# Kernel tuning notes

Hardware: AMD Instinct MI355X
Metric: run time of the kernel (lower is better)

## Reference

```python
import jax, jax.numpy as jnp
import numpy as np

SCALE = 1.0  # std of the Normal error model (init arg `scale`)
B, P, D, T = 32, 256, 64, 4096


def setup_inputs() -> dict:
    key = jax.random.key(0)
    k1, k2, k3 = jax.random.split(key, 3)
    data = jax.random.normal(k1, (B, P, D), dtype=jnp.float32)
    targets = jax.random.normal(k2, (B, P), dtype=jnp.float32)
    task_pool = jax.random.normal(k3, (T, D, 1), dtype=jnp.float32)
    return {"data": data, "targets": targets, "task_pool": task_pool}


def reference(data, targets, task_pool):
    # W: (n_dims, n_tasks), matching task_pool.squeeze(-1).T in the original
    W = task_pool[..., 0].T
    dt = data.dtype

    # Per-point, per-task predictions and Gaussian log-likelihoods, computed ONCE.
    # The original recomputes X@W and the log-prob sum for every prefix i (O(n^2));
    # here a single cumsum over the point axis reproduces the same prefix sums.
    pred_per_task = jnp.einsum('bpd,dt->bpt', data, W)          # (B, P, T)
    err = targets[..., None] - pred_per_task                     # (B, P, T)
    log_norm = -jnp.log(jnp.asarray(SCALE, dt)) - 0.5 * jnp.log(jnp.asarray(2.0 * np.pi, dt))
    scores = -0.5 * (err / SCALE) ** 2 + log_norm                # Normal(0, scale).log_prob

    cum = jnp.cumsum(scores, axis=1)                             # cum[:, i] = sum_{j<=i}
    # Posterior for predicting point i uses points 0..i-1; point 0 uses a uniform
    # posterior (original: W.mean(dim=1) == softmax(zeros) @ W.T).
    log_lik = jnp.concatenate([jnp.zeros_like(cum[:, :1]), cum[:, :-1]], axis=1)
    post = jax.nn.softmax(log_lik, axis=-1)                      # (B, P, T)

    w_mmse = jnp.einsum('bpt,dt->bpd', post, W)                  # posterior-mean weights
    return jnp.einsum('bpd,bpd->bp', data, w_mmse)               # (B, P)
```

## Files before the change

kernel.cpp:

```cpp
#include <hip/hip_runtime.h>
#include <hip/hip_bf16.h>
#include <math.h>

#define Bb 32
#define Pp 256
#define Dd 64
#define Tt 4096

typedef unsigned short ushort_t;
typedef __attribute__((ext_vector_type(8))) short bf16x8;
typedef __attribute__((ext_vector_type(4))) float f32x4;

#define TRIP_BYTES ((size_t)Bb * Pp * 64 * 16)
#define A_BF_BYTES ((size_t)Bb * Pp * Dd * 2)
#define B_BF_BYTES ((size_t)Tt * Dd * 2)
#define WS_NEED    (TRIP_BYTES + 2 * A_BF_BYTES + 2 * B_BF_BYTES)

template <int CTRL>
__device__ __forceinline__ float dppf(float x) {
  return __builtin_bit_cast(float,
      __builtin_amdgcn_update_dpp(0, __builtin_bit_cast(int, x), CTRL, 0xF, 0xF, true));
}

__device__ __forceinline__ f32x4 mfma6(bf16x8 ah0, bf16x8 ah1, bf16x8 al0, bf16x8 al1,
                                       bf16x8 bh0, bf16x8 bh1, bf16x8 bl0, bf16x8 bl1) {
  f32x4 a = (f32x4)0.f;
  a = __builtin_amdgcn_mfma_f32_16x16x32_bf16(ah0, bh0, a, 0, 0, 0);
  a = __builtin_amdgcn_mfma_f32_16x16x32_bf16(ah1, bh1, a, 0, 0, 0);
  a = __builtin_amdgcn_mfma_f32_16x16x32_bf16(ah0, bl0, a, 0, 0, 0);
  a = __builtin_amdgcn_mfma_f32_16x16x32_bf16(al0, bh0, a, 0, 0, 0);
  a = __builtin_amdgcn_mfma_f32_16x16x32_bf16(ah1, bl1, a, 0, 0, 0);
  a = __builtin_amdgcn_mfma_f32_16x16x32_bf16(al1, bh1, a, 0, 0, 0);
  return a;
}

__global__ __launch_bounds__(256) void k_conv(const float* __restrict__ data,
                                              const float* __restrict__ Wt,
                                              ushort_t* __restrict__ Ah, ushort_t* __restrict__ Al,
                                              ushort_t* __restrict__ Bh, ushort_t* __restrict__ Bl) {
  const int i  = blockIdx.x * 256 + threadIdx.x;
  const int NA = Bb * Pp * Dd;
  const float x = (i < NA) ? data[i] : Wt[i - NA];
  const __hip_bfloat16 h = __float2bfloat16(x);
  const float hf = __bfloat162float(h);
  const __hip_bfloat16 l = __float2bfloat16(x - hf);
  if (i < NA) { Ah[i] = *(const ushort_t*)&h; Al[i] = *(const ushort_t*)&l; }
  else        { const int j = i - NA;
                Bh[j] = *(const ushort_t*)&h; Bl[j] = *(const ushort_t*)&l; }
}

__global__ __launch_bounds__(256, 2) void k_main(const ushort_t* __restrict__ Ah,
                                                 const ushort_t* __restrict__ Al,
                                                 const ushort_t* __restrict__ Bh,
                                                 const ushort_t* __restrict__ Bl,
                                                 const float* __restrict__ targets,
                                                 float4* __restrict__ triples) {
  const int tid  = threadIdx.x;
  const int wid  = tid >> 6;
  const int lane = tid & 63;
  const int quad = lane >> 4;
  const int l16  = lane & 15;
  const int b     = blockIdx.x >> 4;
  const int strip = blockIdx.x & 15;
  const int t0    = strip * 256;
  const int wstrip = strip * 4 + wid;

  bf16x8 vbh0[4], vbh1[4], vbl0[4], vbl1[4];
#pragma unroll
  for (int nt = 0; nt < 4; ++nt) {
    const size_t boff = (size_t)(t0 + wid * 64 + nt * 16 + l16) * Dd + quad * 8;
    vbh0[nt] = *(const bf16x8*)(Bh + boff);
    vbh1[nt] = *(const bf16x8*)(Bh + boff + 32);
    vbl0[nt] = *(const bf16x8*)(Bl + boff);
    vbl1[nt] = *(const bf16x8*)(Bl + boff + 32);
  }

  const ushort_t* arow_base = Ah + (size_t)b * Pp * Dd;
  const ushort_t* alow_base = Al + (size_t)b * Pp * Dd;
  float4* __restrict__ trb  = triples + (size_t)b * Pp * 64;

  float R[4];
#pragma unroll
  for (int nt = 0; nt < 4; ++nt) R[nt] = 0.f;

  const size_t aoff0 = (size_t)l16 * Dd + quad * 8;
  bf16x8 ah0 = *(const bf16x8*)(arow_base + aoff0);
  bf16x8 ah1 = *(const bf16x8*)(arow_base + aoff0 + 32);
  bf16x8 al0 = *(const bf16x8*)(alow_base + aoff0);
  bf16x8 al1 = *(const bf16x8*)(alow_base + aoff0 + 32);
  float4 tq  = *(const float4*)(targets + b * Pp + quad * 4);

#pragma unroll 1
  for (int sg = 0; sg < 16; ++sg) {
    const int pn = ((sg + 1) & 15) * 16;
    const size_t an = (size_t)(pn + l16) * Dd + quad * 8;
    const bf16x8 nah0 = *(const bf16x8*)(arow_base + an);
    const bf16x8 nah1 = *(const bf16x8*)(arow_base + an + 32);
    const bf16x8 nal0 = *(const bf16x8*)(alow_base + an);
    const bf16x8 nal1 = *(const bf16x8*)(alow_base + an + 32);
    const float4 ntq  = *(const float4*)(targets + b * Pp + pn + quad * 4);

    float cc[4][4], av[4][4];
#pragma unroll
    for (int nt = 0; nt < 4; ++nt) {
      const f32x4 a = mfma6(ah0, ah1, al0, al1,
                            vbh0[nt], vbh1[nt], vbl0[nt], vbl1[nt]);
      float sc[4];
      { const float e = tq.x - a[0]; sc[0] = -0.5f * e * e; }
      { const float e = tq.y - a[1]; sc[1] = -0.5f * e * e; }
      { const float e = tq.z - a[2]; sc[2] = -0.5f * e * e; }
      { const float e = tq.w - a[3]; sc[3] = -0.5f * e * e; }

      const float colsum = (sc[0] + sc[1]) + (sc[2] + sc[3]);
      const float x1 = __shfl_xor(colsum, 16, 64);
      const float x2 = __shfl_xor(colsum, 32, 64);
      const float x3 = __shfl_xor(x1, 32, 64);
      const float pre = (quad == 0) ? 0.f
                      : (quad == 1) ? x1
                      : (quad == 2) ? (x2 + x3)
                                    : (x1 + x2 + x3);
      const float base = R[nt] + pre;
      cc[nt][0] = base;
      cc[nt][1] = base + sc[0];
      cc[nt][2] = cc[nt][1] + sc[1];
      cc[nt][3] = cc[nt][2] + sc[2];
#pragma unroll
      for (int r = 0; r < 4; ++r) av[nt][r] = a[r];

      R[nt] += ((colsum + x1) + (x2 + x3));
    }

    float mm[4], ss[4], vv[4];
#pragma unroll
    for (int r = 0; r < 4; ++r) {
      const float m01 = fmaxf(cc[0][r], cc[1][r]);
      const float m23 = fmaxf(cc[2][r], cc[3][r]);
      mm[r] = fmaxf(m01, m23);
      float s = 0.f, v = 0.f;
#pragma unroll
      for (int nt = 0; nt < 4; ++nt) {
        const float e = __expf(cc[nt][r] - mm[r]);
        s += e;
        v = fmaf(e, av[nt][r], v);
      }
      ss[r] = s; vv[r] = v;
    }

    float M[4];
#pragma unroll
    for (int r = 0; r < 4; ++r) M[r] = mm[r];
#pragma unroll
    for (int r = 0; r < 4; ++r) M[r] = fmaxf(M[r], dppf<0xB1>(M[r]));
#pragma unroll
    for (int r = 0; r < 4; ++r) M[r] = fmaxf(M[r], dppf<0x4E>(M[r]));
#pragma unroll
    for (int r = 0; r < 4; ++r) M[r] = fmaxf(M[r], dppf<0x141>(M[r]));
#pragma unroll
    for (int r = 0; r < 4; ++r) M[r] = fmaxf(M[r], dppf<0x140>(M[r]));
#pragma unroll
    for (int r = 0; r < 4; ++r) {
      const float f = __expf(mm[r] - M[r]);
      ss[r] *= f; vv[r] *= f;
    }
#pragma unroll
    for (int r = 0; r < 4; ++r) { ss[r] += dppf<0xB1>(ss[r]);  vv[r] += dppf<0xB1>(vv[r]); }
#pragma unroll
    for (int r = 0; r < 4; ++r) { ss[r] += dppf<0x4E>(ss[r]);  vv[r] += dppf<0x4E>(vv[r]); }
#pragma unroll
    for (int r = 0; r < 4; ++r) { ss[r] += dppf<0x141>(ss[r]); vv[r] += dppf<0x141>(vv[r]); }
#pragma unroll
    for (int r = 0; r < 4; ++r) { ss[r] += dppf<0x140>(ss[r]); vv[r] += dppf<0x140>(vv[r]); }

    if (l16 == 0) {
#pragma unroll
      for (int r = 0; r < 4; ++r) {
        const int p = sg * 16 + quad * 4 + r;
        trb[p * 64 + wstrip] = make_float4(M[r], ss[r], vv[r], 0.f);
      }
    }

    ah0 = nah0; ah1 = nah1; al0 = nal0; al1 = nal1; tq = ntq;
  }
}

__global__ __launch_bounds__(256) void k_merge(const float4* __restrict__ ws,
                                               float* __restrict__ out) {
  const int gt   = blockIdx.x * 256 + threadIdx.x;
  const int bp   = gt >> 6;
  const int lane = gt & 63;
  const float4 o = ws[(size_t)bp * 64 + lane];
  const float m = o.x, s = o.y, v = o.z;
  float M = m;
#pragma unroll
  for (int off = 32; off; off >>= 1) M = fmaxf(M, __shfl_xor(M, off, 64));
  const float f = __expf(m - M);
  float S = f * s, V = f * v;
#pragma unroll
  for (int off = 32; off; off >>= 1) {
    S += __shfl_xor(S, off, 64);
    V += __shfl_xor(V, off, 64);
  }
  if (lane == 0) out[bp] = V / S;
}

__global__ __launch_bounds__(256) void k_scan_fused(const float* __restrict__ data,
                                                    const float* __restrict__ targets,
                                                    const float* __restrict__ task_pool,
                                                    float4* __restrict__ ws) {
  const int b     = blockIdx.x >> 4;
  const int wid   = threadIdx.x >> 6;
  const int lane  = threadIdx.x & 63;
  const int chunk = ((blockIdx.x & 15) << 2) | wid;
  const int t     = (chunk << 6) | lane;
  float w[Dd];
#pragma unroll
  for (int d = 0; d < Dd; d += 4) {
    const float4 r = *(const float4*)(task_pool + (size_t)t * Dd + d);
    w[d] = r.x; w[d + 1] = r.y; w[d + 2] = r.z; w[d + 3] = r.w;
  }
  const float* drow = data + (size_t)b * (Pp * Dd);
  const float* tgt  = targets + b * Pp;
  float4* wsb       = ws + (size_t)b * (Pp * 64);
  float c = 0.f;
  for (int p = 0; p < Pp; ++p) {
    float a0 = 0.f, a1 = 0.f, a2 = 0.f, a3 = 0.f;
    const float* r = drow + p * Dd;
#pragma unroll
    for (int d = 0; d < Dd; d += 4) {
      a0 = fmaf(r[d], w[d], a0);         a1 = fmaf(r[d + 1], w[d + 1], a1);
      a2 = fmaf(r[d + 2], w[d + 2], a2); a3 = fmaf(r[d + 3], w[d + 3], a3);
    }
    const float pred = (a0 + a1) + (a2 + a3);
    float m = c;
#pragma unroll
    for (int off = 32; off; off >>= 1) m = fmaxf(m, __shfl_xor(m, off, 64));
    const float e = __expf(c - m);
    float s = e, v = e * pred;
#pragma unroll
    for (int off = 32; off; off >>= 1) {
      s += __shfl_xor(s, off, 64);
      v += __shfl_xor(v, off, 64);
    }
    if (lane == 0) wsb[p * 64 + chunk] = make_float4(m, s, v, 0.f);
    const float err = tgt[p] - pred;
    c = fmaf(-0.5f * err, err, c);
  }
}

extern "C" void kernel_launch(void* const* d_in, const int* in_sizes, int n_in,
                              void* d_out, int out_size, void* d_ws, size_t ws_size,
                              hipStream_t stream) {
  const float* data      = (const float*)d_in[0];
  const float* targets   = (const float*)d_in[1];
  const float* task_pool = (const float*)d_in[2];
  float* out = (float*)d_out;

  if (ws_size >= WS_NEED) {
    float4*   trips = (float4*)d_ws;
    char*     cb    = (char*)d_ws + TRIP_BYTES;
    ushort_t* Ah    = (ushort_t*)cb;
    ushort_t* Al    = (ushort_t*)(cb + A_BF_BYTES);
    ushort_t* Bh    = (ushort_t*)(cb + 2 * A_BF_BYTES);
    ushort_t* Bl    = (ushort_t*)(cb + 2 * A_BF_BYTES + B_BF_BYTES);
    k_conv <<<dim3((Bb * Pp * Dd + Tt * Dd) / 256), dim3(256), 0, stream>>>(
        data, task_pool, Ah, Al, Bh, Bl);
    k_main <<<dim3(Bb * 16), dim3(256), 0, stream>>>(Ah, Al, Bh, Bl, targets, trips);
    k_merge<<<dim3((Bb * Pp * 64) / 256), dim3(256), 0, stream>>>(trips, out);
  } else {
    float4* triples = (float4*)d_ws;
    k_scan_fused<<<dim3(512), dim3(256), 0, stream>>>(data, targets, task_pool, triples);
    k_merge<<<dim3((Bb * Pp * 64) / 256), dim3(256), 0, stream>>>(triples, out);
  }
}
```

Baseline: 101.0 us.

## Fuse bf16 split conversion into main kernel and split point scan across two blocks

Result: slower. 187.9 us (+86.0%).

```diff
diff --git a/kernel.cpp b/kernel.cpp
--- a/kernel.cpp
+++ b/kernel.cpp
@@ -12,9 +12,17 @@
 typedef __attribute__((ext_vector_type(4))) float f32x4;
 
 #define TRIP_BYTES ((size_t)Bb * Pp * 64 * 16)
-#define A_BF_BYTES ((size_t)Bb * Pp * Dd * 2)
-#define B_BF_BYTES ((size_t)Tt * Dd * 2)
-#define WS_NEED    (TRIP_BYTES + 2 * A_BF_BYTES + 2 * B_BF_BYTES)
+#define WS_NEED    TRIP_BYTES
+
+#define C2 (-0.7213475204444817f)
+
+__device__ __forceinline__ float fexp2(float x) {
+#if __has_builtin(__builtin_amdgcn_exp2f)
+  return __builtin_amdgcn_exp2f(x);
+#else
+  float r; asm("v_exp_f32 %0, %1" : "=v"(r) : "v"(x)); return r;
+#endif
+}
 
 template <int CTRL>
 __device__ __forceinline__ float dppf(float x) {
@@ -34,152 +42,177 @@
   return a;
 }
 
-__global__ __launch_bounds__(256) void k_conv(const float* __restrict__ data,
-                                              const float* __restrict__ Wt,
-                                              ushort_t* __restrict__ Ah, ushort_t* __restrict__ Al,
-                                              ushort_t* __restrict__ Bh, ushort_t* __restrict__ Bl) {
-  const int i  = blockIdx.x * 256 + threadIdx.x;
-  const int NA = Bb * Pp * Dd;
-  const float x = (i < NA) ? data[i] : Wt[i - NA];
-  const __hip_bfloat16 h = __float2bfloat16(x);
-  const float hf = __bfloat162float(h);
-  const __hip_bfloat16 l = __float2bfloat16(x - hf);
-  if (i < NA) { Ah[i] = *(const ushort_t*)&h; Al[i] = *(const ushort_t*)&l; }
-  else        { const int j = i - NA;
-                Bh[j] = *(const ushort_t*)&h; Bl[j] = *(const ushort_t*)&l; }
-}
-
-__global__ __launch_bounds__(256, 2) void k_main(const ushort_t* __restrict__ Ah,
-                                                 const ushort_t* __restrict__ Al,
-                                                 const ushort_t* __restrict__ Bh,
-                                                 const ushort_t* __restrict__ Bl,
+__device__ __forceinline__ void cvt8(const float4 a, const float4 b,
+                                     bf16x8* hi, bf16x8* lo) {
+  float f[8] = {a.x, a.y, a.z, a.w, b.x, b.y, b.z, b.w};
+  bf16x8 h, l;
+#pragma unroll
+  for (int j = 0; j < 8; ++j) {
+    const __hip_bfloat16 hb = __float2bfloat16(f[j]);
+    const float hf = __bfloat162float(hb);
+    const __hip_bfloat16 lb = __float2bfloat16(f[j] - hf);
+    h[j] = *(const short*)&hb;
+    l[j] = *(const short*)&lb;
+  }
+  *hi = h; *lo = l;
+}
+
+struct TrueC  { static constexpr bool value = true;  };
+struct FalseC { static constexpr bool value = false; };
+
+#define SPLIT 10
+__global__ __launch_bounds__(256, 4) void k_main(const float* __restrict__ data,
                                                  const float* __restrict__ targets,
+                                                 const float* __restrict__ task_pool,
                                                  float4* __restrict__ triples) {
   const int tid  = threadIdx.x;
   const int wid  = tid >> 6;
   const int lane = tid & 63;
   const int quad = lane >> 4;
   const int l16  = lane & 15;
-  const int b     = blockIdx.x >> 4;
-  const int strip = blockIdx.x & 15;
+  const int b     = blockIdx.x >> 5;
+  const int sub   = blockIdx.x & 31;
+  const int strip = sub >> 1;
+  const int half  = sub & 1;
   const int t0    = strip * 256;
   const int wstrip = strip * 4 + wid;
 
   bf16x8 vbh0[4], vbh1[4], vbl0[4], vbl1[4];
 #pragma unroll
   for (int nt = 0; nt < 4; ++nt) {
-    const size_t boff = (size_t)(t0 + wid * 64 + nt * 16 + l16) * Dd + quad * 8;
-    vbh0[nt] = *(const bf16x8*)(Bh + boff);
-    vbh1[nt] = *(const bf16x8*)(Bh + boff + 32);
-    vbl0[nt] = *(const bf16x8*)(Bl + boff);
-    vbl1[nt] = *(const bf16x8*)(Bl + boff + 32);
-  }
-
-  const ushort_t* arow_base = Ah + (size_t)b * Pp * Dd;
-  const ushort_t* alow_base = Al + (size_t)b * Pp * Dd;
-  float4* __restrict__ trb  = triples + (size_t)b * Pp * 64;
+    const float* wr = task_pool + (size_t)(t0 + wid * 64 + nt * 16 + l16) * Dd + quad * 8;
+    const float4 f0 = *(const float4*)(wr);
+    const float4 f1 = *(const float4*)(wr + 4);
+    const float4 f2 = *(const float4*)(wr + 32);
+    const float4 f3 = *(const float4*)(wr + 36);
+    cvt8(f0, f1, &vbh0[nt], &vbl0[nt]);
+    cvt8(f2, f3, &vbh1[nt], &vbl1[nt]);
+  }
+
+  const float* arow = data + (size_t)b * Pp * Dd;
+  const float* tgt  = targets + b * Pp;
+  float4* __restrict__ trb = triples + (size_t)b * Pp * 64;
 
   float R[4];
 #pragma unroll
   for (int nt = 0; nt < 4; ++nt) R[nt] = 0.f;
 
-  const size_t aoff0 = (size_t)l16 * Dd + quad * 8;
-  bf16x8 ah0 = *(const bf16x8*)(arow_base + aoff0);
-  bf16x8 ah1 = *(const bf16x8*)(arow_base + aoff0 + 32);
-  bf16x8 al0 = *(const bf16x8*)(alow_base + aoff0);
-  bf16x8 al1 = *(const bf16x8*)(alow_base + aoff0 + 32);
-  float4 tq  = *(const float4*)(targets + b * Pp + quad * 4);
-
-#pragma unroll 1
-  for (int sg = 0; sg < 16; ++sg) {
+  bf16x8 ah0, ah1, al0, al1;
+  {
+    const size_t a0 = (size_t)l16 * Dd + quad * 8;
+    const float4 f0 = *(const float4*)(arow + a0);
+    const float4 f1 = *(const float4*)(arow + a0 + 4);
+    const float4 f2 = *(const float4*)(arow + a0 + 32);
+    const float4 f3 = *(const float4*)(arow + a0 + 36);
+    cvt8(f0, f1, &ah0, &al0);
+    cvt8(f2, f3, &ah1, &al1);
+  }
+  float4 tq = *(const float4*)(tgt + quad * 4);
+
+  auto step = [&](auto fullc, int sg) {
+    constexpr bool FULL_ = decltype(fullc)::value;
     const int pn = ((sg + 1) & 15) * 16;
     const size_t an = (size_t)(pn + l16) * Dd + quad * 8;
-    const bf16x8 nah0 = *(const bf16x8*)(arow_base + an);
-    const bf16x8 nah1 = *(const bf16x8*)(arow_base + an + 32);
-    const bf16x8 nal0 = *(const bf16x8*)(alow_base + an);
-    const bf16x8 nal1 = *(const bf16x8*)(alow_base + an + 32);
-    const float4 ntq  = *(const float4*)(targets + b * Pp + pn + quad * 4);
+    const float4 nf0 = *(const float4*)(arow + an);
+    const float4 nf1 = *(const float4*)(arow + an + 4);
+    const float4 nf2 = *(const float4*)(arow + an + 32);
+    const float4 nf3 = *(const float4*)(arow + an + 36);
+    const float4 ntq = *(const float4*)(tgt + pn + quad * 4);
 
     float cc[4][4], av[4][4];
 #pragma unroll
     for (int nt = 0; nt < 4; ++nt) {
       const f32x4 a = mfma6(ah0, ah1, al0, al1,
                             vbh0[nt], vbh1[nt], vbl0[nt], vbl1[nt]);
-      float sc[4];
-      { const float e = tq.x - a[0]; sc[0] = -0.5f * e * e; }
-      { const float e = tq.y - a[1]; sc[1] = -0.5f * e * e; }
-      { const float e = tq.z - a[2]; sc[2] = -0.5f * e * e; }
-      { const float e = tq.w - a[3]; sc[3] = -0.5f * e * e; }
-
-      const float colsum = (sc[0] + sc[1]) + (sc[2] + sc[3]);
+      float sc0, sc1, sc2, sc3;
+      { const float e = tq.x - a[0]; sc0 = C2 * e * e; }
+      { const float e = tq.y - a[1]; sc1 = C2 * e * e; }
+      { const float e = tq.z - a[2]; sc2 = C2 * e * e; }
+      { const float e = tq.w - a[3]; sc3 = C2 * e * e; }
+
+      const float colsum = (sc0 + sc1) + (sc2 + sc3);
       const float x1 = __shfl_xor(colsum, 16, 64);
       const float x2 = __shfl_xor(colsum, 32, 64);
       const float x3 = __shfl_xor(x1, 32, 64);
-      const float pre = (quad == 0) ? 0.f
-                      : (quad == 1) ? x1
-                      : (quad == 2) ? (x2 + x3)
-                                    : (x1 + x2 + x3);
-      const float base = R[nt] + pre;
-      cc[nt][0] = base;
-      cc[nt][1] = base + sc[0];
-      cc[nt][2] = cc[nt][1] + sc[1];
-      cc[nt][3] = cc[nt][2] + sc[2];
-#pragma unroll
-      for (int r = 0; r < 4; ++r) av[nt][r] = a[r];
-
+      if (FULL_) {
+        const float pre = (quad == 0) ? 0.f
+                        : (quad == 1) ? x1
+                        : (quad == 2) ? (x2 + x3)
+                                      : (x1 + x2 + x3);
+        const float base = R[nt] + pre;
+        cc[nt][0] = base;
+        cc[nt][1] = base + sc0;
+        cc[nt][2] = cc[nt][1] + sc1;
+        cc[nt][3] = cc[nt][2] + sc2;
+        av[nt][0] = a[0]; av[nt][1] = a[1]; av[nt][2] = a[2]; av[nt][3] = a[3];
+      }
       R[nt] += ((colsum + x1) + (x2 + x3));
     }
 
-    float mm[4], ss[4], vv[4];
-#pragma unroll
-    for (int r = 0; r < 4; ++r) {
-      const float m01 = fmaxf(cc[0][r], cc[1][r]);
-      const float m23 = fmaxf(cc[2][r], cc[3][r]);
-      mm[r] = fmaxf(m01, m23);
-      float s = 0.f, v = 0.f;
-#pragma unroll
-      for (int nt = 0; nt < 4; ++nt) {
-        const float e = __expf(cc[nt][r] - mm[r]);
-        s += e;
-        v = fmaf(e, av[nt][r], v);
-      }
-      ss[r] = s; vv[r] = v;
-    }
-
-    float M[4];
-#pragma unroll
-    for (int r = 0; r < 4; ++r) M[r] = mm[r];
-#pragma unroll
-    for (int r = 0; r < 4; ++r) M[r] = fmaxf(M[r], dppf<0xB1>(M[r]));
-#pragma unroll
-    for (int r = 0; r < 4; ++r) M[r] = fmaxf(M[r], dppf<0x4E>(M[r]));
-#pragma unroll
-    for (int r = 0; r < 4; ++r) M[r] = fmaxf(M[r], dppf<0x141>(M[r]));
-#pragma unroll
-    for (int r = 0; r < 4; ++r) M[r] = fmaxf(M[r], dppf<0x140>(M[r]));
-#pragma unroll
-    for (int r = 0; r < 4; ++r) {
-      const float f = __expf(mm[r] - M[r]);
-      ss[r] *= f; vv[r] *= f;
-    }
-#pragma unroll
-    for (int r = 0; r < 4; ++r) { ss[r] += dppf<0xB1>(ss[r]);  vv[r] += dppf<0xB1>(vv[r]); }
-#pragma unroll
-    for (int r = 0; r < 4; ++r) { ss[r] += dppf<0x4E>(ss[r]);  vv[r] += dppf<0x4E>(vv[r]); }
-#pragma unroll
-    for (int r = 0; r < 4; ++r) { ss[r] += dppf<0x141>(ss[r]); vv[r] += dppf<0x141>(vv[r]); }
-#pragma unroll
-    for (int r = 0; r < 4; ++r) { ss[r] += dppf<0x140>(ss[r]); vv[r] += dppf<0x140>(vv[r]); }
-
-    if (l16 == 0) {
+    if (FULL_) {
+      float mm[4], ss[4], vv[4];
 #pragma unroll
       for (int r = 0; r < 4; ++r) {
-        const int p = sg * 16 + quad * 4 + r;
-        trb[p * 64 + wstrip] = make_float4(M[r], ss[r], vv[r], 0.f);
-      }
-    }
-
-    ah0 = nah0; ah1 = nah1; al0 = nal0; al1 = nal1; tq = ntq;
+        const float m01 = fmaxf(cc[0][r], cc[1][r]);
+        const float m23 = fmaxf(cc[2][r], cc[3][r]);
+        mm[r] = fmaxf(m01, m23);
+        float s = 0.f, v = 0.f;
+#pragma unroll
+        for (int nt = 0; nt < 4; ++nt) {
+          const float e = fexp2(cc[nt][r] - mm[r]);
+          s += e;
+          v = fmaf(e, av[nt][r], v);
+        }
+        ss[r] = s; vv[r] = v;
+      }
+
+      float M[4];
+#pragma unroll
+      for (int r = 0; r < 4; ++r) M[r] = mm[r];
+#pragma unroll
+      for (int r = 0; r < 4; ++r) M[r] = fmaxf(M[r], dppf<0xB1>(M[r]));
+#pragma unroll
+      for (int r = 0; r < 4; ++r) M[r] = fmaxf(M[r], dppf<0x4E>(M[r]));
+#pragma unroll
+      for (int r = 0; r < 4; ++r) M[r] = fmaxf(M[r], dppf<0x141>(M[r]));
+#pragma unroll
+      for (int r = 0; r < 4; ++r) M[r] = fmaxf(M[r], dppf<0x140>(M[r]));
+#pragma unroll
+      for (int r = 0; r < 4; ++r) {
+        const float f = fexp2(mm[r] - M[r]);
+        ss[r] *= f; vv[r] *= f;
+      }
+#pragma unroll
+      for (int r = 0; r < 4; ++r) { ss[r] += dppf<0xB1>(ss[r]);  vv[r] += dppf<0xB1>(vv[r]); }
+#pragma unroll
+      for (int r = 0; r < 4; ++r) { ss[r] += dppf<0x4E>(ss[r]);  vv[r] += dppf<0x4E>(vv[r]); }
+#pragma unroll
+      for (int r = 0; r < 4; ++r) { ss[r] += dppf<0x141>(ss[r]); vv[r] += dppf<0x141>(vv[r]); }
+#pragma unroll
+      for (int r = 0; r < 4; ++r) { ss[r] += dppf<0x140>(ss[r]); vv[r] += dppf<0x140>(vv[r]); }
+
+      if (l16 == 0) {
+#pragma unroll
+        for (int r = 0; r < 4; ++r) {
+          const int p = sg * 16 + quad * 4 + r;
+          trb[p * 64 + wstrip] = make_float4(M[r], ss[r], vv[r], 0.f);
+        }
+      }
+    }
+
+    cvt8(nf0, nf1, &ah0, &al0);
+    cvt8(nf2, nf3, &ah1, &al1);
+    tq = ntq;
+  };
+
+  if (half == 0) {
+#pragma unroll 1
+    for (int sg = 0; sg < SPLIT; ++sg) step(TrueC{}, sg);
+  } else {
+#pragma unroll 1
+    for (int sg = 0; sg < SPLIT; ++sg) step(FalseC{}, sg);
+#pragma unroll 1
+    for (int sg = SPLIT; sg < 16; ++sg) step(TrueC{}, sg);
   }
 }
 
@@ -193,7 +226,7 @@
   float M = m;
 #pragma unroll
   for (int off = 32; off; off >>= 1) M = fmaxf(M, __shfl_xor(M, off, 64));
-  const float f = __expf(m - M);
+  const float f = fexp2(m - M);
   float S = f * s, V = f * v;
 #pragma unroll
   for (int off = 32; off; off >>= 1) {
@@ -234,7 +267,7 @@
     float m = c;
 #pragma unroll
     for (int off = 32; off; off >>= 1) m = fmaxf(m, __shfl_xor(m, off, 64));
-    const float e = __expf(c - m);
+    const float e = fexp2(c - m);
     float s = e, v = e * pred;
 #pragma unroll
     for (int off = 32; off; off >>= 1) {
@@ -243,7 +276,7 @@
     }
     if (lane == 0) wsb[p * 64 + chunk] = make_float4(m, s, v, 0.f);
     const float err = tgt[p] - pred;
-    c = fmaf(-0.5f * err, err, c);
+    c = fmaf(C2 * err, err, c);
   }
 }
 
@@ -255,20 +288,12 @@
   const float* task_pool = (const float*)d_in[2];
   float* out = (float*)d_out;
 
+  float4* trips = (float4*)d_ws;
   if (ws_size >= WS_NEED) {
-    float4*   trips = (float4*)d_ws;
-    char*     cb    = (char*)d_ws + TRIP_BYTES;
-    ushort_t* Ah    = (ushort_t*)cb;
-    ushort_t* Al    = (ushort_t*)(cb + A_BF_BYTES);
-    ushort_t* Bh    = (ushort_t*)(cb + 2 * A_BF_BYTES);
-    ushort_t* Bl    = (ushort_t*)(cb + 2 * A_BF_BYTES + B_BF_BYTES);
-    k_conv <<<dim3((Bb * Pp * Dd + Tt * Dd) / 256), dim3(256), 0, stream>>>(
-        data, task_pool, Ah, Al, Bh, Bl);
-    k_main <<<dim3(Bb * 16), dim3(256), 0, stream>>>(Ah, Al, Bh, Bl, targets, trips);
+    k_main <<<dim3(Bb * 32), dim3(256), 0, stream>>>(data, targets, task_pool, trips);
     k_merge<<<dim3((Bb * Pp * 64) / 256), dim3(256), 0, stream>>>(trips, out);
   } else {
-    float4* triples = (float4*)d_ws;
-    k_scan_fused<<<dim3(512), dim3(256), 0, stream>>>(data, targets, task_pool, triples);
-    k_merge<<<dim3((Bb * Pp * 64) / 256), dim3(256), 0, stream>>>(triples, out);
-  }
-}
+    k_scan_fused<<<dim3(512), dim3(256), 0, stream>>>(data, targets, task_pool, trips);
+    k_merge<<<dim3((Bb * Pp * 64) / 256), dim3(256), 0, stream>>>(trips, out);
+  }
+}
```

## Split point scan across two blocks with redundant prefix recompute; use base-2 exp

Applied to the files above, without the earlier changes.

Measured after the change: 179.0 us. 77.2% more time.

```diff
diff --git a/kernel.cpp b/kernel.cpp
--- a/kernel.cpp
+++ b/kernel.cpp
@@ -15,6 +15,12 @@
 #define A_BF_BYTES ((size_t)Bb * Pp * Dd * 2)
 #define B_BF_BYTES ((size_t)Tt * Dd * 2)
 #define WS_NEED    (TRIP_BYTES + 2 * A_BF_BYTES + 2 * B_BF_BYTES)
+
+#define C2 (-0.7213475204444817f)
+
+__device__ __forceinline__ float fexp2(float x) {
+  float r; asm("v_exp_f32 %0, %1" : "=v"(r) : "v"(x)); return r;
+}
 
 template <int CTRL>
 __device__ __forceinline__ float dppf(float x) {
@@ -49,7 +55,110 @@
                 Bh[j] = *(const ushort_t*)&h; Bl[j] = *(const ushort_t*)&l; }
 }
 
-__global__ __launch_bounds__(256, 2) void k_main(const ushort_t* __restrict__ Ah,
+#define SPLIT 10
+
+template <bool FULL>
+__device__ __forceinline__ void step_fn(
+    int sg, int quad, int l16, int wstrip,
+    const ushort_t* __restrict__ arow_base, const ushort_t* __restrict__ alow_base,
+    const float* __restrict__ tgt, float4* __restrict__ trb,
+    bf16x8& ah0, bf16x8& ah1, bf16x8& al0, bf16x8& al1, float4& tq,
+    float (&R)[4],
+    const bf16x8 (&vbh0)[4], const bf16x8 (&vbh1)[4],
+    const bf16x8 (&vbl0)[4], const bf16x8 (&vbl1)[4]) {
+  const int pn = ((sg + 1) & 15) * 16;
+  const size_t an = (size_t)(pn + l16) * Dd + quad * 8;
+  const bf16x8 nah0 = *(const bf16x8*)(arow_base + an);
+  const bf16x8 nah1 = *(const bf16x8*)(arow_base + an + 32);
+  const bf16x8 nal0 = *(const bf16x8*)(alow_base + an);
+  const bf16x8 nal1 = *(const bf16x8*)(alow_base + an + 32);
+  const float4 ntq  = *(const float4*)(tgt + pn + quad * 4);
+
+  float cc[4][4], av[4][4];
+#pragma unroll
+  for (int nt = 0; nt < 4; ++nt) {
+    const f32x4 a = mfma6(ah0, ah1, al0, al1,
+                          vbh0[nt], vbh1[nt], vbl0[nt], vbl1[nt]);
+    float sc0, sc1, sc2, sc3;
+    { const float e = tq.x - a[0]; sc0 = C2 * e * e; }
+    { const float e = tq.y - a[1]; sc1 = C2 * e * e; }
+    { const float e = tq.z - a[2]; sc2 = C2 * e * e; }
+    { const float e = tq.w - a[3]; sc3 = C2 * e * e; }
+
+    const float colsum = (sc0 + sc1) + (sc2 + sc3);
+    const float x1 = __shfl_xor(colsum, 16, 64);
+    const float x2 = __shfl_xor(colsum, 32, 64);
+    const float x3 = __shfl_xor(x1, 32, 64);
+    if (FULL) {
+      const float pre = (quad == 0) ? 0.f
+                      : (quad == 1) ? x1
+                      : (quad == 2) ? (x2 + x3)
+                                    : (x1 + x2 + x3);
+      const float base = R[nt] + pre;
+      cc[nt][0] = base;
+      cc[nt][1] = base + sc0;
+      cc[nt][2] = cc[nt][1] + sc1;
+      cc[nt][3] = cc[nt][2] + sc2;
+      av[nt][0] = a[0]; av[nt][1] = a[1]; av[nt][2] = a[2]; av[nt][3] = a[3];
+    }
+    R[nt] += ((colsum + x1) + (x2 + x3));
+  }
+
+  if (FULL) {
+    float mm[4], ss[4], vv[4];
+#pragma unroll
+    for (int r = 0; r < 4; ++r) {
+      const float m01 = fmaxf(cc[0][r], cc[1][r]);
+      const float m23 = fmaxf(cc[2][r], cc[3][r]);
+      mm[r] = fmaxf(m01, m23);
+      float s = 0.f, v = 0.f;
+#pragma unroll
+      for (int nt = 0; nt < 4; ++nt) {
+        const float e = fexp2(cc[nt][r] - mm[r]);
+        s += e;
+        v = fmaf(e, av[nt][r], v);
+      }
+      ss[r] = s; vv[r] = v;
+    }
+
+    float M[4];
+#pragma unroll
+    for (int r = 0; r < 4; ++r) M[r] = mm[r];
+#pragma unroll
+    for (int r = 0; r < 4; ++r) M[r] = fmaxf(M[r], dppf<0xB1>(M[r]));
+#pragma unroll
+    for (int r = 0; r < 4; ++r) M[r] = fmaxf(M[r], dppf<0x4E>(M[r]));
+#pragma unroll
+    for (int r = 0; r < 4; ++r) M[r] = fmaxf(M[r], dppf<0x141>(M[r]));
+#pragma unroll
+    for (int r = 0; r < 4; ++r) M[r] = fmaxf(M[r], dppf<0x140>(M[r]));
+#pragma unroll
+    for (int r = 0; r < 4; ++r) {
+      const float f = fexp2(mm[r] - M[r]);
+      ss[r] *= f; vv[r] *= f;
+    }
+#pragma unroll
+    for (int r = 0; r < 4; ++r) { ss[r] += dppf<0xB1>(ss[r]);  vv[r] += dppf<0xB1>(vv[r]); }
+#pragma unroll
+    for (int r = 0; r < 4; ++r) { ss[r] += dppf<0x4E>(ss[r]);  vv[r] += dppf<0x4E>(vv[r]); }
+#pragma unroll
+    for (int r = 0; r < 4; ++r) { ss[r] += dppf<0x141>(ss[r]); vv[r] += dppf<0x141>(vv[r]); }
+#pragma unroll
+    for (int r = 0; r < 4; ++r) { ss[r] += dppf<0x140>(ss[r]); vv[r] += dppf<0x140>(vv[r]); }
+
+    if (l16 == 0) {
+#pragma unroll
+      for (int r = 0; r < 4; ++r) {
+        const int p = sg * 16 + quad * 4 + r;
+        trb[p * 64 + wstrip] = make_float4(M[r], ss[r], vv[r], 0.f);
+      }
+    }
+  }
+
+  ah0 = nah0; ah1 = nah1; al0 = nal0; al1 = nal1; tq = ntq;
+}
+
+__global__ __launch_bounds__(256, 4) void k_main(const ushort_t* __restrict__ Ah,
                                                  const ushort_t* __restrict__ Al,
                                                  const ushort_t* __restrict__ Bh,
                                                  const ushort_t* __restrict__ Bl,
@@ -60,8 +169,10 @@
   const int lane = tid & 63;
   const int quad = lane >> 4;
   const int l16  = lane & 15;
-  const int b     = blockIdx.x >> 4;
-  const int strip = blockIdx.x & 15;
+  const int b     = blockIdx.x >> 5;
+  const int sub   = blockIdx.x & 31;
+  const int strip = sub >> 1;
+  const int half  = sub & 1;
   const int t0    = strip * 256;
   const int wstrip = strip * 4 + wid;
 
@@ -77,6 +188,7 @@
 
   const ushort_t* arow_base = Ah + (size_t)b * Pp * Dd;
   const ushort_t* alow_base = Al + (size_t)b * Pp * Dd;
+  const float* tgt          = targets + b * Pp;
   float4* __restrict__ trb  = triples + (size_t)b * Pp * 64;
 
   float R[4];
@@ -88,98 +200,22 @@
   bf16x8 ah1 = *(const bf16x8*)(arow_base + aoff0 + 32);
   bf16x8 al0 = *(const bf16x8*)(alow_base + aoff0);
   bf16x8 al1 = *(const bf16x8*)(alow_base + aoff0 + 32);
-  float4 tq  = *(const float4*)(targets + b * Pp + quad * 4);
-
+  float4 tq  = *(const float4*)(tgt + quad * 4);
+
+  if (half == 0) {
 #pragma unroll 1
-  for (int sg = 0; sg < 16; ++sg) {
-    const int pn = ((sg + 1) & 15) * 16;
-    const size_t an = (size_t)(pn + l16) * Dd + quad * 8;
-    const bf16x8 nah0 = *(const bf16x8*)(arow_base + an);
-    const bf16x8 nah1 = *(const bf16x8*)(arow_base + an + 32);
-    const bf16x8 nal0 = *(const bf16x8*)(alow_base + an);
-    const bf16x8 nal1 = *(const bf16x8*)(alow_base + an + 32);
-    const float4 ntq  = *(const float4*)(targets + b * Pp + pn + quad * 4);
-
-    float cc[4][4], av[4][4];
-#pragma unroll
-    for (int nt = 0; nt < 4; ++nt) {
-      const f32x4 a = mfma6(ah0, ah1, al0, al1,
-                            vbh0[nt], vbh1[nt], vbl0[nt], vbl1[nt]);
-      float sc[4];
-      { const float e = tq.x - a[0]; sc[0] = -0.5f * e * e; }
-      { const float e = tq.y - a[1]; sc[1] = -0.5f * e * e; }
-      { const float e = tq.z - a[2]; sc[2] = -0.5f * e * e; }
-      { const float e = tq.w - a[3]; sc[3] = -0.5f * e * e; }
-
-      const float colsum = (sc[0] + sc[1]) + (sc[2] + sc[3]);
-      const float x1 = __shfl_xor(colsum, 16, 64);
-      const float x2 = __shfl_xor(colsum, 32, 64);
-      const float x3 = __shfl_xor(x1, 32, 64);
-      const float pre = (quad == 0) ? 0.f
-                      : (quad == 1) ? x1
-                      : (quad == 2) ? (x2 + x3)
-                                    : (x1 + x2 + x3);
-      const float base = R[nt] + pre;
-      cc[nt][0] = base;
-      cc[nt][1] = base + sc[0];
-      cc[nt][2] = cc[nt][1] + sc[1];
-      cc[nt][3] = cc[nt][2] + sc[2];
-#pragma unroll
-      for (int r = 0; r < 4; ++r) av[nt][r] = a[r];
-
-      R[nt] += ((colsum + x1) + (x2 + x3));
-    }
-
-    float mm[4], ss[4], vv[4];
-#pragma unroll
-    for (int r = 0; r < 4; ++r) {
-      const float m01 = fmaxf(cc[0][r], cc[1][r]);
-      const float m23 = fmaxf(cc[2][r], cc[3][r]);
-      mm[r] = fmaxf(m01, m23);
-      float s = 0.f, v = 0.f;
-#pragma unroll
-      for (int nt = 0; nt < 4; ++nt) {
-        const float e = __expf(cc[nt][r] - mm[r]);
-        s += e;
-        v = fmaf(e, av[nt][r], v);
-      }
-      ss[r] = s; vv[r] = v;
-    }
-
-    float M[4];
-#pragma unroll
-    for (int r = 0; r < 4; ++r) M[r] = mm[r];
-#pragma unroll
-    for (int r = 0; r < 4; ++r) M[r] = fmaxf(M[r], dppf<0xB1>(M[r]));
-#pragma unroll
-    for (int r = 0; r < 4; ++r) M[r] = fmaxf(M[r], dppf<0x4E>(M[r]));
-#pragma unroll
-    for (int r = 0; r < 4; ++r) M[r] = fmaxf(M[r], dppf<0x141>(M[r]));
-#pragma unroll
-    for (int r = 0; r < 4; ++r) M[r] = fmaxf(M[r], dppf<0x140>(M[r]));
-#pragma unroll
-    for (int r = 0; r < 4; ++r) {
-      const float f = __expf(mm[r] - M[r]);
-      ss[r] *= f; vv[r] *= f;
-    }
-#pragma unroll
-    for (int r = 0; r < 4; ++r) { ss[r] += dppf<0xB1>(ss[r]);  vv[r] += dppf<0xB1>(vv[r]); }
-#pragma unroll
-    for (int r = 0; r < 4; ++r) { ss[r] += dppf<0x4E>(ss[r]);  vv[r] += dppf<0x4E>(vv[r]); }
-#pragma unroll
-    for (int r = 0; r < 4; ++r) { ss[r] += dppf<0x141>(ss[r]); vv[r] += dppf<0x141>(vv[r]); }
-#pragma unroll
-    for (int r = 0; r < 4; ++r) { ss[r] += dppf<0x140>(ss[r]); vv[r] += dppf<0x140>(vv[r]); }
-
-    if (l16 == 0) {
-#pragma unroll
-      for (int r = 0; r < 4; ++r) {
-        const int p = sg * 16 + quad * 4 + r;
-        trb[p * 64 + wstrip] = make_float4(M[r], ss[r], vv[r], 0.f);
-      }
-    }
-
-    ah0 = nah0; ah1 = nah1; al0 = nal0; al1 = nal1; tq = ntq;
+    for (int sg = 0; sg < SPLIT; ++sg)
+      step_fn<true>(sg, quad, l16, wstrip, arow_base, alow_base, tgt, trb,
+                    ah0, ah1, al0, al1, tq, R, vbh0, vbh1, vbl0, vbl1);
+  } else {
+#pragma unroll 1
+    for (int sg = 0; sg < SPLIT; ++sg)
+      step_fn<false>(sg, quad, l16, wstrip, arow_base, alow_base, tgt, trb,
+                     ah0, ah1, al0, al1, tq, R, vbh0, vbh1, vbl0, vbl1);
+#pragma unroll 1
+    for (int sg = SPLIT; sg < 16; ++sg)
+      step_fn<true>(sg, quad, l16, wstrip, arow_base, alow_base, tgt, trb,
+                    ah0, ah1, al0, al1, tq, R, vbh0, vbh1, vbl0, vbl1);
   }
 }
 
@@ -193,7 +229,7 @@
   float M = m;
 #pragma unroll
   for (int off = 32; off; off >>= 1) M = fmaxf(M, __shfl_xor(M, off, 64));
-  const float f = __expf(m - M);
+  const float f = fexp2(m - M);
   float S = f * s, V = f * v;
 #pragma unroll
   for (int off = 32; off; off >>= 1) {
@@ -234,7 +270,7 @@
     float m = c;
 #pragma unroll
     for (int off = 32; off; off >>= 1) m = fmaxf(m, __shfl_xor(m, off, 64));
-    const float e = __expf(c - m);
+    const float e = fexp2(c - m);
     float s = e, v = e * pred;
 #pragma unroll
     for (int off = 32; off; off >>= 1) {
@@ -243,7 +279,7 @@
     }
     if (lane == 0) wsb[p * 64 + chunk] = make_float4(m, s, v, 0.f);
     const float err = tgt[p] - pred;
-    c = fmaf(-0.5f * err, err, c);
+    c = fmaf(C2 * err, err, c);
   }
 }
 
@@ -264,7 +300,7 @@
     ushort_t* Bl    = (ushort_t*)(cb + 2 * A_BF_BYTES + B_BF_BYTES);
     k_conv <<<dim3((Bb * Pp * Dd + Tt * Dd) / 256), dim3(256), 0, stream>>>(
         data, task_pool, Ah, Al, Bh, Bl);
-    k_main <<<dim3(Bb * 16), dim3(256), 0, stream>>>(Ah, Al, Bh, Bl, targets, trips);
+    k_main <<<dim3(Bb * 32), dim3(256), 0, stream>>>(Ah, Al, Bh, Bl, targets, trips);
     k_merge<<<dim3((Bb * Pp * 64) / 256), dim3(256), 0, stream>>>(trips, out);
   } else {
     float4* triples = (float4*)d_ws;
```

## Halve per-wave task strip, double blocks, compress partials to log-sum-exp pairs

Applied to the files above, without the earlier changes.

Result: slower. 106.8 us (+5.7%).

```diff
diff --git a/kernel.cpp b/kernel.cpp
--- a/kernel.cpp
+++ b/kernel.cpp
@@ -11,10 +11,22 @@
 typedef __attribute__((ext_vector_type(8))) short bf16x8;
 typedef __attribute__((ext_vector_type(4))) float f32x4;
 
-#define TRIP_BYTES ((size_t)Bb * Pp * 64 * 16)
+#define TRIP_BYTES ((size_t)Bb * Pp * 128 * 8)
 #define A_BF_BYTES ((size_t)Bb * Pp * Dd * 2)
 #define B_BF_BYTES ((size_t)Tt * Dd * 2)
 #define WS_NEED    (TRIP_BYTES + 2 * A_BF_BYTES + 2 * B_BF_BYTES)
+
+#define C2 (-0.7213475204444817f)
+
+__device__ __forceinline__ float fexp2(float x) {
+  float r; asm("v_exp_f32 %0, %1" : "=v"(r) : "v"(x)); return r;
+}
+__device__ __forceinline__ float flog2(float x) {
+  float r; asm("v_log_f32 %0, %1" : "=v"(r) : "v"(x)); return r;
+}
+__device__ __forceinline__ float frcp(float x) {
+  float r; asm("v_rcp_f32 %0, %1" : "=v"(r) : "v"(x)); return r;
+}
 
 template <int CTRL>
 __device__ __forceinline__ float dppf(float x) {
@@ -49,69 +61,64 @@
                 Bh[j] = *(const ushort_t*)&h; Bl[j] = *(const ushort_t*)&l; }
 }
 
-__global__ __launch_bounds__(256, 2) void k_main(const ushort_t* __restrict__ Ah,
+__global__ __launch_bounds__(256, 4) void k_main(const ushort_t* __restrict__ Ah,
                                                  const ushort_t* __restrict__ Al,
                                                  const ushort_t* __restrict__ Bh,
                                                  const ushort_t* __restrict__ Bl,
                                                  const float* __restrict__ targets,
-                                                 float4* __restrict__ triples) {
+                                                 float2* __restrict__ trips) {
   const int tid  = threadIdx.x;
   const int wid  = tid >> 6;
   const int lane = tid & 63;
   const int quad = lane >> 4;
   const int l16  = lane & 15;
-  const int b     = blockIdx.x >> 4;
-  const int strip = blockIdx.x & 15;
-  const int t0    = strip * 256;
+  const int b     = blockIdx.x >> 5;
+  const int strip = blockIdx.x & 31;
+  const int t0    = strip * 128;
   const int wstrip = strip * 4 + wid;
 
-  bf16x8 vbh0[4], vbh1[4], vbl0[4], vbl1[4];
-#pragma unroll
-  for (int nt = 0; nt < 4; ++nt) {
-    const size_t boff = (size_t)(t0 + wid * 64 + nt * 16 + l16) * Dd + quad * 8;
-    vbh0[nt] = *(const bf16x8*)(Bh + boff);
-    vbh1[nt] = *(const bf16x8*)(Bh + boff + 32);
-    vbl0[nt] = *(const bf16x8*)(Bl + boff);
-    vbl1[nt] = *(const bf16x8*)(Bl + boff + 32);
+  bf16x8 b0h0, b0h1, b0l0, b0l1, b1h0, b1h1, b1l0, b1l1;
+  {
+    const size_t r0 = (size_t)(t0 + wid * 32 + l16) * Dd + quad * 8;
+    b0h0 = *(const bf16x8*)(Bh + r0);
+    b0h1 = *(const bf16x8*)(Bh + r0 + 32);
+    b0l0 = *(const bf16x8*)(Bl + r0);
+    b0l1 = *(const bf16x8*)(Bl + r0 + 32);
+    const size_t r1 = r0 + (size_t)16 * Dd;
+    b1h0 = *(const bf16x8*)(Bh + r1);
+    b1h1 = *(const bf16x8*)(Bh + r1 + 32);
+    b1l0 = *(const bf16x8*)(Bl + r1);
+    b1l1 = *(const bf16x8*)(Bl + r1 + 32);
   }
 
   const ushort_t* arow_base = Ah + (size_t)b * Pp * Dd;
   const ushort_t* alow_base = Al + (size_t)b * Pp * Dd;
-  float4* __restrict__ trb  = triples + (size_t)b * Pp * 64;
-
-  float R[4];
-#pragma unroll
-  for (int nt = 0; nt < 4; ++nt) R[nt] = 0.f;
-
-  const size_t aoff0 = (size_t)l16 * Dd + quad * 8;
-  bf16x8 ah0 = *(const bf16x8*)(arow_base + aoff0);
-  bf16x8 ah1 = *(const bf16x8*)(arow_base + aoff0 + 32);
-  bf16x8 al0 = *(const bf16x8*)(alow_base + aoff0);
-  bf16x8 al1 = *(const bf16x8*)(alow_base + aoff0 + 32);
-  float4 tq  = *(const float4*)(targets + b * Pp + quad * 4);
+  const float* tgt          = targets + b * Pp;
+  float2* __restrict__ trb  = trips + (size_t)b * Pp * 128;
+
+  float R0 = 0.f, R1 = 0.f;
 
 #pragma unroll 1
   for (int sg = 0; sg < 16; ++sg) {
-    const int pn = ((sg + 1) & 15) * 16;
-    const size_t an = (size_t)(pn + l16) * Dd + quad * 8;
-    const bf16x8 nah0 = *(const bf16x8*)(arow_base + an);
-    const bf16x8 nah1 = *(const bf16x8*)(arow_base + an + 32);
-    const bf16x8 nal0 = *(const bf16x8*)(alow_base + an);
-    const bf16x8 nal1 = *(const bf16x8*)(alow_base + an + 32);
-    const float4 ntq  = *(const float4*)(targets + b * Pp + pn + quad * 4);
-
-    float cc[4][4], av[4][4];
-#pragma unroll
-    for (int nt = 0; nt < 4; ++nt) {
-      const f32x4 a = mfma6(ah0, ah1, al0, al1,
-                            vbh0[nt], vbh1[nt], vbl0[nt], vbl1[nt]);
-      float sc[4];
-      { const float e = tq.x - a[0]; sc[0] = -0.5f * e * e; }
-      { const float e = tq.y - a[1]; sc[1] = -0.5f * e * e; }
-      { const float e = tq.z - a[2]; sc[2] = -0.5f * e * e; }
-      { const float e = tq.w - a[3]; sc[3] = -0.5f * e * e; }
-
-      const float colsum = (sc[0] + sc[1]) + (sc[2] + sc[3]);
+    const int p0 = sg * 16;
+    const size_t aoff = (size_t)(p0 + l16) * Dd + quad * 8;
+    const bf16x8 ah0 = *(const bf16x8*)(arow_base + aoff);
+    const bf16x8 ah1 = *(const bf16x8*)(arow_base + aoff + 32);
+    const bf16x8 al0 = *(const bf16x8*)(alow_base + aoff);
+    const bf16x8 al1 = *(const bf16x8*)(alow_base + aoff + 32);
+    const float4 tq  = *(const float4*)(tgt + p0 + quad * 4);
+
+    const f32x4 a0 = mfma6(ah0, ah1, al0, al1, b0h0, b0h1, b0l0, b0l1);
+    const f32x4 a1 = mfma6(ah0, ah1, al0, al1, b1h0, b1h1, b1l0, b1l1);
+
+    float cc0_0, cc0_1, cc0_2, cc0_3, cc1_0, cc1_1, cc1_2, cc1_3;
+    {
+      float s0, s1, s2, s3;
+      { const float e = tq.x - a0[0]; s0 = C2 * e * e; }
+      { const float e = tq.y - a0[1]; s1 = C2 * e * e; }
+      { const float e = tq.z - a0[2]; s2 = C2 * e * e; }
+      { const float e = tq.w - a0[3]; s3 = C2 * e * e; }
+      const float colsum = (s0 + s1) + (s2 + s3);
       const float x1 = __shfl_xor(colsum, 16, 64);
       const float x2 = __shfl_xor(colsum, 32, 64);
       const float x3 = __shfl_xor(x1, 32, 64);
@@ -119,82 +126,100 @@
                       : (quad == 1) ? x1
                       : (quad == 2) ? (x2 + x3)
                                     : (x1 + x2 + x3);
-      const float base = R[nt] + pre;
-      cc[nt][0] = base;
-      cc[nt][1] = base + sc[0];
-      cc[nt][2] = cc[nt][1] + sc[1];
-      cc[nt][3] = cc[nt][2] + sc[2];
-#pragma unroll
-      for (int r = 0; r < 4; ++r) av[nt][r] = a[r];
-
-      R[nt] += ((colsum + x1) + (x2 + x3));
-    }
-
-    float mm[4], ss[4], vv[4];
-#pragma unroll
-    for (int r = 0; r < 4; ++r) {
-      const float m01 = fmaxf(cc[0][r], cc[1][r]);
-      const float m23 = fmaxf(cc[2][r], cc[3][r]);
-      mm[r] = fmaxf(m01, m23);
-      float s = 0.f, v = 0.f;
-#pragma unroll
-      for (int nt = 0; nt < 4; ++nt) {
-        const float e = __expf(cc[nt][r] - mm[r]);
-        s += e;
-        v = fmaf(e, av[nt][r], v);
+      const float base = R0 + pre;
+      cc0_0 = base;
+      cc0_1 = base + s0;
+      cc0_2 = cc0_1 + s1;
+      cc0_3 = cc0_2 + s2;
+      R0 += ((colsum + x1) + (x2 + x3));
+    }
+    {
+      float s0, s1, s2, s3;
+      { const float e = tq.x - a1[0]; s0 = C2 * e * e; }
+      { const float e = tq.y - a1[1]; s1 = C2 * e * e; }
+      { const float e = tq.z - a1[2]; s2 = C2 * e * e; }
+      { const float e = tq.w - a1[3]; s3 = C2 * e * e; }
+      const float colsum = (s0 + s1) + (s2 + s3);
+      const float x1 = __shfl_xor(colsum, 16, 64);
+      const float x2 = __shfl_xor(colsum, 32, 64);
+      const float x3 = __shfl_xor(x1, 32, 64);
+      const float pre = (quad == 0) ? 0.f
+                      : (quad == 1) ? x1
+                      : (quad == 2) ? (x2 + x3)
+                                    : (x1 + x2 + x3);
+      const float base = R1 + pre;
+      cc1_0 = base;
+      cc1_1 = base + s0;
+      cc1_2 = cc1_1 + s1;
+      cc1_3 = cc1_2 + s2;
+      R1 += ((colsum + x1) + (x2 + x3));
+    }
+
+    float M[4];
+    M[0] = fmaxf(cc0_0, cc1_0);
+    M[1] = fmaxf(cc0_1, cc1_1);
+    M[2] = fmaxf(cc0_2, cc1_2);
+    M[3] = fmaxf(cc0_3, cc1_3);
+#pragma unroll
+    for (int r = 0; r < 4; ++r) M[r] = fmaxf(M[r], dppf<0xB1>(M[r]));
+#pragma unroll
+    for (int r = 0; r < 4; ++r) M[r] = fmaxf(M[r], dppf<0x4E>(M[r]));
+#pragma unroll
+    for (int r = 0; r < 4; ++r) M[r] = fmaxf(M[r], dppf<0x141>(M[r]));
+#pragma unroll
+    for (int r = 0; r < 4; ++r) M[r] = fmaxf(M[r], dppf<0x140>(M[r]));
+
+    float ss[4], vv[4];
+    {
+      const float e0 = fexp2(cc0_0 - M[0]), e1 = fexp2(cc1_0 - M[0]);
+      ss[0] = e0 + e1; vv[0] = fmaf(e0, a0[0], e1 * a1[0]);
+    }
+    {
+      const float e0 = fexp2(cc0_1 - M[1]), e1 = fexp2(cc1_1 - M[1]);
+      ss[1] = e0 + e1; vv[1] = fmaf(e0, a0[1], e1 * a1[1]);
+    }
+    {
+      const float e0 = fexp2(cc0_2 - M[2]), e1 = fexp2(cc1_2 - M[2]);
+      ss[2] = e0 + e1; vv[2] = fmaf(e0, a0[2], e1 * a1[2]);
+    }
+    {
+      const float e0 = fexp2(cc0_3 - M[3]), e1 = fexp2(cc1_3 - M[3]);
+      ss[3] = e0 + e1; vv[3] = fmaf(e0, a0[3], e1 * a1[3]);
+    }
+
+#pragma unroll
+    for (int r = 0; r < 4; ++r) { ss[r] += dppf<0xB1>(ss[r]);  vv[r] += dppf<0xB1>(vv[r]); }
+#pragma unroll
+    for (int r = 0; r < 4; ++r) { ss[r] += dppf<0x4E>(ss[r]);  vv[r] += dppf<0x4E>(vv[r]); }
+#pragma unroll
+    for (int r = 0; r < 4; ++r) { ss[r] += dppf<0x141>(ss[r]); vv[r] += dppf<0x141>(vv[r]); }
+#pragma unroll
+    for (int r = 0; r < 4; ++r) { ss[r] += dppf<0x140>(ss[r]); vv[r] += dppf<0x140>(vv[r]); }
+
+    if (l16 == 0) {
+#pragma unroll
+      for (int r = 0; r < 4; ++r) {
+        const float lm = M[r] + flog2(ss[r]);
+        const float u  = vv[r] * frcp(ss[r]);
+        const int p = p0 + quad * 4 + r;
+        trb[p * 128 + wstrip] = make_float2(lm, u);
       }
-      ss[r] = s; vv[r] = v;
-    }
-
-    float M[4];
-#pragma unroll
-    for (int r = 0; r < 4; ++r) M[r] = mm[r];
-#pragma unroll
-    for (int r = 0; r < 4; ++r) M[r] = fmaxf(M[r], dppf<0xB1>(M[r]));
-#pragma unroll
-    for (int r = 0; r < 4; ++r) M[r] = fmaxf(M[r], dppf<0x4E>(M[r]));
-#pragma unroll
-    for (int r = 0; r < 4; ++r) M[r] = fmaxf(M[r], dppf<0x141>(M[r]));
-#pragma unroll
-    for (int r = 0; r < 4; ++r) M[r] = fmaxf(M[r], dppf<0x140>(M[r]));
-#pragma unroll
-    for (int r = 0; r < 4; ++r) {
-      const float f = __expf(mm[r] - M[r]);
-      ss[r] *= f; vv[r] *= f;
-    }
-#pragma unroll
-    for (int r = 0; r < 4; ++r) { ss[r] += dppf<0xB1>(ss[r]);  vv[r] += dppf<0xB1>(vv[r]); }
-#pragma unroll
-    for (int r = 0; r < 4; ++r) { ss[r] += dppf<0x4E>(ss[r]);  vv[r] += dppf<0x4E>(vv[r]); }
-#pragma unroll
-    for (int r = 0; r < 4; ++r) { ss[r] += dppf<0x141>(ss[r]); vv[r] += dppf<0x141>(vv[r]); }
-#pragma unroll
-    for (int r = 0; r < 4; ++r) { ss[r] += dppf<0x140>(ss[r]); vv[r] += dppf<0x140>(vv[r]); }
-
-    if (l16 == 0) {
-#pragma unroll
-      for (int r = 0; r < 4; ++r) {
-        const int p = sg * 16 + quad * 4 + r;
-        trb[p * 64 + wstrip] = make_float4(M[r], ss[r], vv[r], 0.f);
-      }
-    }
-
-    ah0 = nah0; ah1 = nah1; al0 = nal0; al1 = nal1; tq = ntq;
-  }
-}
-
-__global__ __launch_bounds__(256) void k_merge(const float4* __restrict__ ws,
+    }
+  }
+}
+
+__global__ __launch_bounds__(256) void k_merge(const float2* __restrict__ ws,
                                                float* __restrict__ out) {
-  const int gt   = blockIdx.x * 256 + threadIdx.x;
-  const int bp   = gt >> 6;
-  const int lane = gt & 63;
-  const float4 o = ws[(size_t)bp * 64 + lane];
-  const float m = o.x, s = o.y, v = o.z;
-  float M = m;
+  const int bp   = blockIdx.x * 4 + (threadIdx.x >> 6);
+  const int lane = threadIdx.x & 63;
+  const float2 e0 = ws[(size_t)bp * 128 + lane];
+  const float2 e1 = ws[(size_t)bp * 128 + 64 + lane];
+  float M = fmaxf(e0.x, e1.x);
 #pragma unroll
   for (int off = 32; off; off >>= 1) M = fmaxf(M, __shfl_xor(M, off, 64));
-  const float f = __expf(m - M);
-  float S = f * s, V = f * v;
+  const float f0 = fexp2(e0.x - M), f1 = fexp2(e1.x - M);
+  float S = f0 + f1;
+  float V = fmaf(f0, e0.y, f1 * e1.y);
 #pragma unroll
   for (int off = 32; off; off >>= 1) {
     S += __shfl_xor(S, off, 64);
@@ -206,7 +231,7 @@
 __global__ __launch_bounds__(256) void k_scan_fused(const float* __restrict__ data,
                                                     const float* __restrict__ targets,
                                                     const float* __restrict__ task_pool,
-                                                    float4* __restrict__ ws) {
+                                                    float2* __restrict__ ws) {
   const int b     = blockIdx.x >> 4;
   const int wid   = threadIdx.x >> 6;
   const int lane  = threadIdx.x & 63;
@@ -220,7 +245,7 @@
   }
   const float* drow = data + (size_t)b * (Pp * Dd);
   const float* tgt  = targets + b * Pp;
-  float4* wsb       = ws + (size_t)b * (Pp * 64);
+  float2* wsb       = ws + (size_t)b * (Pp * 128);
   float c = 0.f;
   for (int p = 0; p < Pp; ++p) {
     float a0 = 0.f, a1 = 0.f, a2 = 0.f, a3 = 0.f;
@@ -234,16 +259,19 @@
     float m = c;
 #pragma unroll
     for (int off = 32; off; off >>= 1) m = fmaxf(m, __shfl_xor(m, off, 64));
-    const float e = __expf(c - m);
+    const float e = fexp2(c - m);
     float s = e, v = e * pred;
 #pragma unroll
     for (int off = 32; off; off >>= 1) {
       s += __shfl_xor(s, off, 64);
       v += __shfl_xor(v, off, 64);
     }
-    if (lane == 0) wsb[p * 64 + chunk] = make_float4(m, s, v, 0.f);
+    if (lane == 0) {
+      wsb[p * 128 + chunk]      = make_float2(m + flog2(s), v * frcp(s));
+      wsb[p * 128 + 64 + chunk] = make_float2(-1e30f, 0.f);
+    }
     const float err = tgt[p] - pred;
-    c = fmaf(-0.5f * err, err, c);
+    c = fmaf(C2 * err, err, c);
   }
 }
 
@@ -256,7 +284,7 @@
   float* out = (float*)d_out;
 
   if (ws_size >= WS_NEED) {
-    float4*   trips = (float4*)d_ws;
+    float2*   trips = (float2*)d_ws;
     char*     cb    = (char*)d_ws + TRIP_BYTES;
     ushort_t* Ah    = (ushort_t*)cb;
     ushort_t* Al    = (ushort_t*)(cb + A_BF_BYTES);
@@ -264,11 +292,11 @@
     ushort_t* Bl    = (ushort_t*)(cb + 2 * A_BF_BYTES + B_BF_BYTES);
     k_conv <<<dim3((Bb * Pp * Dd + Tt * Dd) / 256), dim3(256), 0, stream>>>(
         data, task_pool, Ah, Al, Bh, Bl);
-    k_main <<<dim3(Bb * 16), dim3(256), 0, stream>>>(Ah, Al, Bh, Bl, targets, trips);
-    k_merge<<<dim3((Bb * Pp * 64) / 256), dim3(256), 0, stream>>>(trips, out);
+    k_main <<<dim3(Bb * 32), dim3(256), 0, stream>>>(Ah, Al, Bh, Bl, targets, trips);
+    k_merge<<<dim3((Bb * Pp) / 4), dim3(256), 0, stream>>>(trips, out);
   } else {
-    float4* triples = (float4*)d_ws;
-    k_scan_fused<<<dim3(512), dim3(256), 0, stream>>>(data, targets, task_pool, triples);
-    k_merge<<<dim3((Bb * Pp * 64) / 256), dim3(256), 0, stream>>>(triples, out);
-  }
-}
+    float2* trips = (float2*)d_ws;
+    k_scan_fused<<<dim3(512), dim3(256), 0, stream>>>(data, targets, task_pool, trips);
+    k_merge<<<dim3((Bb * Pp) / 4), dim3(256), 0, stream>>>(trips, out);
+  }
+}
```
